# Optimization experiments

Hardware: AMD Instinct MI355X
Metric: run time of the kernel (lower is better)

## Reference

```python
import jax, jax.numpy as jnp
from jax import lax
import numpy as np

B, C2, H2, W2 = 16, 512, 28, 28
C3, H3, W3 = 1024, 14, 14
N_CORESET, EMB = 16384, C2 + C3
IMG = 224
NUM_NEIGHBORS = 9
SIGMA = 4.0
KS = 2 * int(4.0 * SIGMA + 0.5) + 1  # kornia default kernel size = 33


def setup_inputs() -> dict:
    key = jax.random.key(0)
    k1, k2, k3 = jax.random.split(key, 3)
    return {
        "feat_layer2": jax.random.normal(k1, (B, C2, H2, W2), jnp.float32),
        "feat_layer3": jax.random.normal(k2, (B, C3, H3, W3), jnp.float32),
        "embedding_coreset": jax.random.normal(k3, (N_CORESET, EMB), jnp.float32),
    }


def avg_pool3(x):
    # torch.nn.AvgPool2d(3, 1, 1), count_include_pad=True -> always divide by 9
    s = lax.reduce_window(x, 0.0, lax.add, (1, 1, 3, 3), (1, 1, 1, 1),
                          [(0, 0), (0, 0), (1, 1), (1, 1)])
    return s / 9.0


def cdist(a, b):
    # euclidean cdist: [Q,E] x [N,E] -> [Q,N]
    a2 = jnp.sum(a * a, axis=-1, keepdims=True)          # [Q,1]
    b2 = jnp.sum(b * b, axis=-1)[None, :]                # [1,N]
    d2 = a2 + b2 - 2.0 * (a @ b.T)
    return jnp.sqrt(jnp.maximum(d2, 1e-12))


def gaussian_blur(x):
    # kornia GaussianBlur2d(kernel=33, sigma=4, border='reflect'), separable
    half = (KS - 1) // 2
    t = jnp.arange(KS, dtype=x.dtype) - half
    k = jnp.exp(-(t * t) / (2.0 * SIGMA * SIGMA))
    k = k / jnp.sum(k)
    xp = jnp.pad(x, ((0, 0), (0, 0), (half, half), (half, half)), mode="reflect")
    dn = ("NCHW", "OIHW", "NCHW")
    y = lax.conv_general_dilated(xp, k.reshape(1, 1, KS, 1), (1, 1), "VALID", dimension_numbers=dn)
    y = lax.conv_general_dilated(y, k.reshape(1, 1, 1, KS), (1, 1), "VALID", dimension_numbers=dn)
    return y


def reference(feat_layer2, feat_layer3, embedding_coreset):
    # 1. feature pooling (AvgPool2d(3,1,1)) on each backbone layer
    p2 = avg_pool3(feat_layer2)                           # [B,512,28,28]
    p3 = avg_pool3(feat_layer3)                           # [B,1024,14,14]
    p3u = jnp.repeat(jnp.repeat(p3, 2, axis=2), 2, axis=3)  # [B,1024,28,28]
    embedding = jnp.concatenate([p2, p3u], axis=1)        # [B,1536,28,28]
    b, e, w, h = embedding.shape
    x = embedding.transpose(0, 2, 3, 1).reshape(-1, e)    # [B*28*28, 1536]

    # 3. nearest neighbor (n_neighbors=1) against the coreset
    dists = cdist(x, embedding_coreset)                   # [Q, N]
    patch_scores = jnp.min(dists, axis=1).reshape(b, -1)  # [B, P]
    locations = jnp.argmin(dists, axis=1).reshape(b, -1)  # [B, P]

    # 4. image-level anomaly score with num_neighbors=9 reweighting
    bidx = jnp.arange(b)
    max_patches = jnp.argmax(patch_scores, axis=1)        # [B]
    mpf = x.reshape(b, w * h, e)[bidx, max_patches]       # [B, E]
    score = patch_scores[bidx, max_patches]               # [B]
    nn_index = locations[bidx, max_patches]               # [B]
    nn_sample = embedding_coreset[nn_index]               # [B, E]
    d2 = cdist(nn_sample, embedding_coreset)              # [B, N]
    _, support = lax.top_k(-d2, NUM_NEIGHBORS)            # smallest 9, ascending
    sup_feats = embedding_coreset[support]                # [B, 9, E]
    diff = mpf[:, None, :] - sup_feats
    d_sup = jnp.sqrt(jnp.maximum(jnp.sum(diff * diff, axis=-1), 1e-12))  # [B, 9]
    weights = (1.0 - jax.nn.softmax(d_sup, axis=1))[:, 0]
    anomaly_score = weights * score                       # [B]

    # 5. anomaly map: bilinear upsample + gaussian blur
    sm = patch_scores.reshape(b, 1, w, h)
    sm = jax.image.resize(sm, (b, 1, IMG, IMG), method="bilinear")
    anomaly_map = gaussian_blur(sm)                       # [B,1,224,224]
    return anomaly_map, anomaly_score
```

## Files before the change

kernel.cpp:

```cpp
#include <hip/hip_runtime.h>
#include <math.h>

typedef unsigned char u8;
typedef unsigned short u16;
typedef unsigned int u32;
typedef unsigned long long u64;
typedef __attribute__((ext_vector_type(8))) int int8v;
typedef __attribute__((ext_vector_type(4))) int int4v;
typedef __attribute__((ext_vector_type(4))) float f32x4;

#define B_IMG 16
#define EMB 1536
#define NPATCH 784
#define Q_TOT (B_IMG * NPATCH)
#define NCORE 16384
#define BK 128
#define IMG 224
#define KS 33
#define HALF 16
#define REFINE_W 12.0f

#define BM 256
#define BN 256
#define MBLK (Q_TOT / BM)
#define NBLK2 (NCORE / BN)
#define NHALF 256
#define NKS (EMB / BK)


__device__ __forceinline__ u32 fkey(float f) {
    u32 u = __float_as_uint(f);
    return (u & 0x80000000u) ? ~u : (u | 0x80000000u);
}
__device__ __forceinline__ float fkey_inv(u32 k) {
    u32 u = (k & 0x80000000u) ? (k ^ 0x80000000u) : ~k;
    return __uint_as_float(u);
}

__device__ __forceinline__ u32 f2e4m3(float f) {
    u32 x = __float_as_uint(f);
    u32 sign = (x >> 24) & 0x80u;
    x &= 0x7fffffffu;
    if (x >= 0x43E00000u) return sign | 0x7Eu;
    u32 e = x >> 23;
    if (e >= 121) {
        u32 m = x & 0x7fffffu;
        u32 keep = m >> 20;
        u32 rest = m & 0xFFFFFu;
        u32 rnd = (rest > 0x80000u) || (rest == 0x80000u && (keep & 1u));
        u32 mant = keep + rnd;
        u32 e4 = e - 120;
        if (mant == 8) { mant = 0; e4 += 1; }
        return sign | (e4 << 3) | mant;
    }
    float a = __uint_as_float(x);
    u32 q = (u32)(a * 512.0f + 0.5f);
    if (q > 7) return sign | 0x08u;
    return sign | q;
}

__device__ __forceinline__ void async_copy16(const void* gsrc, void* ldst) {
    auto g = reinterpret_cast<const __attribute__((address_space(1))) u32*>(
        reinterpret_cast<uintptr_t>(gsrc));
    auto l = reinterpret_cast<__attribute__((address_space(3))) u32*>(
        reinterpret_cast<uintptr_t>(ldst));
    __builtin_amdgcn_global_load_lds(g, l, 16, 0, 0);
}

__global__ void k_split_cs(const float* __restrict__ cs, u8* __restrict__ cs8,
                           float* __restrict__ b2) {
    __shared__ float sm[4];
    const int n = blockIdx.x;
    const int t = threadIdx.x;
    const size_t base = (size_t)n * EMB;
    float s = 0.f;
#pragma unroll
    for (int i = 0; i < 6; ++i) {
        const int e = t + i * 256;
        float v = cs[base + e];
        cs8[base + e] = (u8)f2e4m3(v);
        s += v * v;
    }
#pragma unroll
    for (int off = 32; off > 0; off >>= 1) s += __shfl_down(s, off, 64);
    if ((t & 63) == 0) sm[t >> 6] = s;
    __syncthreads();
    if (t == 0) b2[n] = sm[0] + sm[1] + sm[2] + sm[3];
}

__global__ void k_build_x(const float* __restrict__ f2, const float* __restrict__ f3,
                          u8* __restrict__ x8, float* __restrict__ xf) {
    __shared__ float tile[32][33];
    const int tx = threadIdx.x, ty = threadIdx.y;
    const int hw0 = blockIdx.x * 32;
    const int e0 = blockIdx.y * 32;
    const int b = blockIdx.z;
    const int hw = hw0 + tx;
    const bool ok = hw < NPATCH;
    const int h = hw / 28, w = hw - h * 28;
#pragma unroll
    for (int j = 0; j < 4; ++j) {
        const int el = ty + 8 * j;
        const int e = e0 + el;
        float v = 0.f;
        if (ok) {
            if (e < 512) {
                const float* p = f2 + (size_t)(b * 512 + e) * 784;
#pragma unroll
                for (int dy = -1; dy <= 1; ++dy) {
                    int yy = h + dy;
                    if (yy < 0 || yy >= 28) continue;
#pragma unroll
                    for (int dx = -1; dx <= 1; ++dx) {
                        int xx = w + dx;
                        if (xx < 0 || xx >= 28) continue;
                        v += p[yy * 28 + xx];
                    }
                }
            } else {
                const int c = e - 512;
                const int y3 = h >> 1, x3 = w >> 1;
                const float* p = f3 + (size_t)(b * 1024 + c) * 196;
#pragma unroll
                for (int dy = -1; dy <= 1; ++dy) {
                    int yy = y3 + dy;
                    if (yy < 0 || yy >= 14) continue;
#pragma unroll
                    for (int dx = -1; dx <= 1; ++dx) {
                        int xx = x3 + dx;
                        if (xx < 0 || xx >= 14) continue;
                        v += p[yy * 14 + xx];
                    }
                }
            }
            v *= (1.0f / 9.0f);
        }
        tile[el][tx] = v;
    }
    __syncthreads();
#pragma unroll
    for (int j = 0; j < 4; ++j) {
        const int hwl = ty + 8 * j;
        const int hw2 = hw0 + hwl;
        if (hw2 < NPATCH) {
            const int q = b * NPATCH + hw2;
            const float v = tile[tx][hwl];
            x8[(size_t)q * EMB + e0 + tx] = (u8)f2e4m3(v);
            xf[(size_t)q * EMB + e0 + tx] = v;
        }
    }
}

__global__ __launch_bounds__(512, 2) void k_gemm(
    const u8* __restrict__ x8, const u8* __restrict__ cs8,
    const float* __restrict__ b2, u64* __restrict__ cand) {
    __shared__ __align__(16) u8 sA0[BM * BK];
    __shared__ __align__(16) u8 sA1[BM * BK];
    __shared__ __align__(16) u8 sB0[BN * BK];
    __shared__ __align__(16) u8 sB1[BN * BK];

    const int tid = threadIdx.x;
    const int lane = tid & 63;
    const int wid = tid >> 6;
    const int wy = wid >> 2;
    const int wx = wid & 3;
    const int qd = lane >> 4;
    const int lr = lane & 15;
    const int sw = lr & 7;

    const u32 bid = blockIdx.x;
    const u32 xcd = bid & 7;
    const u32 sl = bid >> 3;
    const int bx = (int)(xcd * 8 + (sl & 7));
    const int by = (int)(sl >> 3);
    const int m0 = by * BM;
    const int n0 = bx * BN;

    size_t srcA[4], srcB[4];
    int dst[4];
#pragma unroll
    for (int j = 0; j < 4; ++j) {
        const int s = tid + j * 512;
        const int r = s >> 3, p = s & 7;
        const int col = (p ^ (r & 7)) << 4;
        srcA[j] = (size_t)(m0 + r) * EMB + col;
        srcB[j] = (size_t)(n0 + r) * EMB + col;
        dst[j] = s << 4;
    }

    f32x4 acc[8][4];
#pragma unroll
    for (int i = 0; i < 8; ++i)
#pragma unroll
        for (int j = 0; j < 4; ++j) acc[i][j] = (f32x4){0.f, 0.f, 0.f, 0.f};

    const int aoff0 = (wy * 128 + lr) * BK + (((qd * 2) ^ sw) << 4);
    const int boff0 = (wx * 64 + lr) * BK + (((qd * 2) ^ sw) << 4);

#define STAGE(SA, SB, KSI) do {                                                \
        const size_t kk_ = (size_t)(KSI) * BK;                                 \
        _Pragma("unroll")                                                      \
        for (int j_ = 0; j_ < 4; ++j_) {                                       \
            async_copy16(x8 + srcA[j_] + kk_, (SA) + dst[j_]);                 \
            async_copy16(cs8 + srcB[j_] + kk_, (SB) + dst[j_]);                \
        }                                                                      \
    } while (0)

#define COMPUTE(SA, SB) do {                                                   \
        int8v a_[8];                                                           \
        _Pragma("unroll")                                                      \
        for (int mi_ = 0; mi_ < 8; ++mi_) {                                    \
            const int o_ = aoff0 + mi_ * (16 * BK);                            \
            *(int4v*)&a_[mi_] = *(const int4v*)((SA) + o_);                    \
            *(((int4v*)&a_[mi_]) + 1) = *(const int4v*)((SA) + (o_ ^ 16));     \
        }                                                                      \
        _Pragma("unroll")                                                      \
        for (int nj_ = 0; nj_ < 4; ++nj_) {                                    \
            const int ob_ = boff0 + nj_ * (16 * BK);                           \
            int8v b_;                                                          \
            *(int4v*)&b_ = *(const int4v*)((SB) + ob_);                        \
            *(((int4v*)&b_) + 1) = *(const int4v*)((SB) + (ob_ ^ 16));         \
            _Pragma("unroll")                                                  \
            for (int mi_ = 0; mi_ < 8; ++mi_)                                  \
                acc[mi_][nj_] = __builtin_amdgcn_mfma_scale_f32_16x16x128_f8f6f4( \
                    a_[mi_], b_, acc[mi_][nj_], 0, 0, 0, 0x7F7F7F7F, 0, 0x7F7F7F7F); \
        }                                                                      \
    } while (0)

    STAGE(sA0, sB0, 0);
    __syncthreads();
    for (int ks = 0; ks < NKS; ks += 2) {
        STAGE(sA1, sB1, ks + 1);
        COMPUTE(sA0, sB0);
        __syncthreads();
        if (ks + 2 < NKS) STAGE(sA0, sB0, ks + 2);
        COMPUTE(sA1, sB1);
        __syncthreads();
    }
#undef STAGE
#undef COMPUTE

    float bb[4];
#pragma unroll
    for (int nj = 0; nj < 4; ++nj) bb[nj] = b2[n0 + wx * 64 + nj * 16 + lr];

#pragma unroll
    for (int mi = 0; mi < 8; ++mi) {
#pragma unroll
        for (int r = 0; r < 4; ++r) {
            u64 best = ~0ull;
#pragma unroll
            for (int nj = 0; nj < 4; ++nj) {
                const int n_g = n0 + wx * 64 + nj * 16 + lr;
                float v = bb[nj] - 2.0f * acc[mi][nj][r];
                u64 key = ((u64)fkey(v) << 32) | (u32)n_g;
                best = best < key ? best : key;
            }
#pragma unroll
            for (int s = 1; s < 16; s <<= 1) {
                u64 o = __shfl_xor(best, s, 64);
                best = best < o ? best : o;
            }
            if (lr == 0) {
                const int m_l = wy * 128 + mi * 16 + qd * 4 + r;
                cand[(size_t)(m0 + m_l) * NHALF + (bx * 4 + wx)] = best;
            }
        }
    }
}

__global__ void k_refine(const u64* __restrict__ cand, const float* __restrict__ xf,
                         const float* __restrict__ cs,
                         float* __restrict__ scores, int* __restrict__ locs) {
    __shared__ float sx[EMB];
    __shared__ float wred_f[4];
    __shared__ u64 wred_u[4];
    __shared__ u64 wbest_s[4];
    __shared__ int clist[16];
    __shared__ int ccount;
    __shared__ float s_a2, s_lim;
    const int row = blockIdx.x;
    const int t = threadIdx.x;
    const int lane = t & 63, wv = t >> 6;

    const u64 mykey = cand[(size_t)row * NHALF + t];
    float p = 0.f;
    for (int e = t; e < EMB; e += 256) {
        float v = xf[(size_t)row * EMB + e];
        sx[e] = v;
        p += v * v;
    }
    if (t == 0) ccount = 0;
#pragma unroll
    for (int off = 32; off > 0; off >>= 1) p += __shfl_down(p, off, 64);
    u64 kmin = mykey;
#pragma unroll
    for (int s = 1; s < 64; s <<= 1) {
        u64 o = __shfl_xor(kmin, s, 64);
        kmin = o < kmin ? o : kmin;
    }
    if (lane == 0) { wred_f[wv] = p; wred_u[wv] = kmin; }
    __syncthreads();
    if (t == 0) {
        float a2 = wred_f[0] + wred_f[1] + wred_f[2] + wred_f[3];
        u64 km = wred_u[0];
        km = wred_u[1] < km ? wred_u[1] : km;
        km = wred_u[2] < km ? wred_u[2] : km;
        km = wred_u[3] < km ? wred_u[3] : km;
        s_a2 = a2;
        s_lim = a2 + fkey_inv((u32)(km >> 32)) + REFINE_W;
    }
    __syncthreads();
    {
        float d2a = s_a2 + fkey_inv((u32)(mykey >> 32));
        if (d2a <= s_lim) {
            int pos = atomicAdd(&ccount, 1);
            if (pos < 16) clist[pos] = (int)(mykey & 0xffffffffu);
        }
    }
    __syncthreads();
    const int nc = min(ccount, 16);
    u64 wb = ~0ull;
    for (int i = wv; i < nc; i += 4) {
        const int n = clist[i];
        const float* c = cs + (size_t)n * EMB;
        float q = 0.f;
        for (int e = lane; e < EMB; e += 64) {
            float d = sx[e] - c[e];
            q += d * d;
        }
#pragma unroll
        for (int off = 32; off > 0; off >>= 1) q += __shfl_down(q, off, 64);
        if (lane == 0) {
            u64 key = ((u64)fkey(q) << 32) | (u32)n;
            wb = wb < key ? wb : key;
        }
    }
    if (lane == 0) wbest_s[wv] = wb;
    __syncthreads();
    if (t == 0) {
        u64 best = wbest_s[0];
        best = wbest_s[1] < best ? wbest_s[1] : best;
        best = wbest_s[2] < best ? wbest_s[2] : best;
        best = wbest_s[3] < best ? wbest_s[3] : best;
        float d2 = fkey_inv((u32)(best >> 32));
        scores[row] = sqrtf(fmaxf(d2, 1e-12f));
        locs[row] = (int)(best & 0xffffffffu);
    }
}

__global__ void k_argmax(const float* __restrict__ scores, const int* __restrict__ locs,
                         float* __restrict__ imgscore, int* __restrict__ nnidx,
                         int* __restrict__ qstar) {
    __shared__ u64 red[4];
    const int b = blockIdx.x, t = threadIdx.x;
    const int lane = t & 63, wv = t >> 6;
    u64 best = 0;
    for (int p = t; p < NPATCH; p += 256) {
        u32 u = __float_as_uint(scores[b * NPATCH + p]);
        u64 key = ((u64)u << 32) | (u32)(0xFFFFFFFFu - (u32)p);
        best = best > key ? best : key;
    }
#pragma unroll
    for (int s = 1; s < 64; s <<= 1) {
        u64 o = __shfl_xor(best, s, 64);
        best = o > best ? o : best;
    }
    if (lane == 0) red[wv] = best;
    __syncthreads();
    if (t == 0) {
        u64 k = red[0];
        k = red[1] > k ? red[1] : k;
        k = red[2] > k ? red[2] : k;
        k = red[3] > k ? red[3] : k;
        int p = (int)(0xFFFFFFFFu - (u32)(k & 0xFFFFFFFFu));
        imgscore[b] = __uint_as_float((u32)(k >> 32));
        nnidx[b] = locs[b * NPATCH + p];
        qstar[b] = b * NPATCH + p;
    }
}

__global__ void k_d2nn(const float* __restrict__ cs, const int* __restrict__ nnidx,
                       float* __restrict__ dpart) {
    __shared__ float snn[16 * 384];
    const int t = threadIdx.x;
    const int nb = blockIdx.x & 63, ksl = blockIdx.x >> 6;
    const int n = nb * 256 + t;
    const int k0 = ksl * 384;
#pragma unroll
    for (int j = 0; j < 6; ++j) {
        int fid = t + j * 256;
        int row = fid / 96;
        int c4 = fid - row * 96;
        ((float4*)snn)[row * 96 + c4] =
            ((const float4*)(cs + (size_t)nnidx[row] * EMB + k0))[c4];
    }
    __syncthreads();
    float acc[16];
#pragma unroll
    for (int b = 0; b < 16; ++b) acc[b] = 0.f;
    const float4* csrow = (const float4*)(cs + (size_t)n * EMB + k0);
    for (int k4 = 0; k4 < 96; ++k4) {
        float4 c4 = csrow[k4];
#pragma unroll
        for (int b = 0; b < 16; ++b) {
            float4 nb4 = ((const float4*)snn)[b * 96 + k4];
            acc[b] += c4.x * nb4.x + c4.y * nb4.y + c4.z * nb4.z + c4.w * nb4.w;
        }
    }
#pragma unroll
    for (int b = 0; b < 16; ++b)
        dpart[((size_t)ksl * 16 + b) * NCORE + n] = acc[b];
}

__global__ void k_topk(const float* __restrict__ dpart, const float* __restrict__ b2,
                       const int* __restrict__ nnidx,
                       const float* __restrict__ cs, const float* __restrict__ xf,
                       const int* __restrict__ qstar, const float* __restrict__ imgscore,
                       float* __restrict__ out_scores) {
    __shared__ float sd2[NCORE];
    __shared__ float sxq[EMB];
    __shared__ int sel_idx[9];
    __shared__ float dsup[9];
    __shared__ u64 wred[4];
    const int b = blockIdx.x, t = threadIdx.x;
    const int lane = t & 63, wv = t >> 6;
    const float bnn = b2[nnidx[b]];
    const int q = qstar[b];
    for (int n = t; n < NCORE; n += 256) {
        float dot = dpart[(0 * 16 + b) * NCORE + n] + dpart[(1 * 16 + b) * NCORE + n] +
                    dpart[(2 * 16 + b) * NCORE + n] + dpart[(3 * 16 + b) * NCORE + n];
        sd2[n] = bnn + b2[n] - 2.f * dot;
    }
    for (int e = t; e < EMB; e += 256) sxq[e] = xf[(size_t)q * EMB + e];
    __syncthreads();

    for (int j = 0; j < 9; ++j) {
        u64 best = ~0ull;
        for (int n = t; n < NCORE; n += 256) {
            u64 key = ((u64)fkey(sd2[n]) << 32) | (u32)n;
            best = best < key ? best : key;
        }
#pragma unroll
        for (int s = 1; s < 64; s <<= 1) {
            u64 o = __shfl_xor(best, s, 64);
            best = o < best ? o : best;
        }
        if (lane == 0) wred[wv] = best;
        __syncthreads();
        if (t == 0) {
            u64 k0 = wred[0];
            k0 = wred[1] < k0 ? wred[1] : k0;
            k0 = wred[2] < k0 ? wred[2] : k0;
            k0 = wred[3] < k0 ? wred[3] : k0;
            int sel = (int)(k0 & 0xffffffffu);
            sel_idx[j] = sel;
            sd2[sel] = __uint_as_float(0x7F800000u);
        }
        __syncthreads();
    }

    for (int j = wv; j < 9; j += 4) {
        const int s = sel_idx[j];
        const float* c = cs + (size_t)s * EMB;
        float p = 0.f;
        for (int e = lane; e < EMB; e += 64) {
            float d = sxq[e] - c[e];
            p += d * d;
        }
#pragma unroll
        for (int off = 32; off > 0; off >>= 1) p += __shfl_down(p, off, 64);
        if (lane == 0) dsup[j] = sqrtf(fmaxf(p, 1e-12f));
    }
    __syncthreads();

    if (t == 0) {
        float m = dsup[0];
        for (int j = 1; j < 9; ++j) m = fmaxf(m, dsup[j]);
        float se = 0.f, e0 = 0.f;
        for (int j = 0; j < 9; ++j) {
            float e = expf(dsup[j] - m);
            se += e;
            if (j == 0) e0 = e;
        }
        out_scores[b] = (1.0f - e0 / se) * imgscore[b];
    }
}

__global__ void k_bilx(const float* __restrict__ scores, float* __restrict__ Sx) {
    int i = blockIdx.x * 256 + threadIdx.x;
    if (i >= B_IMG * 28 * IMG) return;
    int x = i % IMG;
    int br = i / IMG;
    int r = br % 28, b = br / 28;
    float cx = (x + 0.5f) * 0.125f - 0.5f;
    int x0 = (int)floorf(cx);
    float fx = cx - (float)x0;
    int x1 = min(max(x0 + 1, 0), 27);
    x0 = min(max(x0, 0), 27);
    const float* s = scores + b * NPATCH + r * 28;
    Sx[i] = (1.f - fx) * s[x0] + fx * s[x1];
}

__global__ void k_blur_vf(const float* __restrict__ Sx, float* __restrict__ out1) {
    __shared__ float wv[28];
    const int y = blockIdx.x, b = blockIdx.y, t = threadIdx.x;
    if (t < 28) wv[t] = 0.f;
    __syncthreads();
    if (t == 0) {
        float wsum = 0.f;
        for (int j = 0; j < KS; ++j) {
            float d = (float)(j - HALF);
            wsum += expf(-(d * d) / 32.0f);
        }
        for (int j = 0; j < KS; ++j) {
            int yy = y - HALF + j;
            yy = yy < 0 ? -yy : (yy > 223 ? 446 - yy : yy);
            float cy = (yy + 0.5f) * 0.125f - 0.5f;
            int y0 = (int)floorf(cy);
            float fy = cy - (float)y0;
            int y1 = min(max(y0 + 1, 0), 27);
            y0 = min(max(y0, 0), 27);
            float d = (float)(j - HALF);
            float wkj = expf(-(d * d) / 32.0f) / wsum;
            wv[y0] += (1.f - fy) * wkj;
            wv[y1] += fy * wkj;
        }
    }
    __syncthreads();
    if (t < IMG) {
        float acc = 0.f;
#pragma unroll
        for (int r = 0; r < 28; ++r) acc += wv[r] * Sx[(b * 28 + r) * IMG + t];
        out1[((size_t)b * IMG + y) * IMG + t] = acc;
    }
}

__global__ void k_blur_h(const float* __restrict__ out1, float* __restrict__ out) {
    __shared__ float row[IMG];
    __shared__ float wk[KS];
    const int y = blockIdx.x, b = blockIdx.y, t = threadIdx.x;
    if (t < IMG) row[t] = out1[((size_t)b * IMG + y) * IMG + t];
    if (t < KS) {
        float d = (float)(t - HALF);
        wk[t] = expf(-(d * d) / 32.0f);
    }
    __syncthreads();
    if (t < IMG) {
        float wsum = 0.f, acc = 0.f;
#pragma unroll
        for (int j = 0; j < KS; ++j) wsum += wk[j];
#pragma unroll
        for (int j = 0; j < KS; ++j) {
            int xx = t - HALF + j;
            xx = xx < 0 ? -xx : (xx > 223 ? 446 - xx : xx);
            acc += wk[j] * row[xx];
        }
        out[((size_t)b * IMG + y) * IMG + t] = acc / wsum;
    }
}

extern "C" void kernel_launch(void* const* d_in, const int* in_sizes, int n_in,
                              void* d_out, int out_size, void* d_ws, size_t ws_size,
                              hipStream_t stream) {
    const float* f2 = (const float*)d_in[0];
    const float* f3 = (const float*)d_in[1];
    const float* cs = (const float*)d_in[2];
    float* out = (float*)d_out;

    char* w = (char*)d_ws;
    auto alloc = [&](size_t bytes) {
        char* p = w;
        w += (bytes + 255) & ~(size_t)255;
        return p;
    };
    u8* x8 = (u8*)alloc((size_t)Q_TOT * EMB);
    float* xf = (float*)alloc((size_t)Q_TOT * EMB * 4);
    u8* cs8 = (u8*)alloc((size_t)NCORE * EMB);
    float* b2 = (float*)alloc(NCORE * 4);
    u64* cand = (u64*)alloc((size_t)Q_TOT * NHALF * 8);
    float* scores = (float*)alloc(Q_TOT * 4);
    int* locs = (int*)alloc(Q_TOT * 4);
    float* imgscore = (float*)alloc(B_IMG * 4);
    int* nnidx = (int*)alloc(B_IMG * 4);
    int* qstar = (int*)alloc(B_IMG * 4);
    float* dpart = (float*)alloc((size_t)4 * B_IMG * NCORE * 4);
    float* Sx = (float*)alloc((size_t)B_IMG * 28 * IMG * 4);
    float* map1 = (float*)alloc((size_t)B_IMG * IMG * IMG * 4);

    k_split_cs<<<NCORE, 256, 0, stream>>>(cs, cs8, b2);
    k_build_x<<<dim3(25, 48, 16), dim3(32, 8), 0, stream>>>(f2, f3, x8, xf);
    k_gemm<<<dim3(MBLK * NBLK2), 512, 0, stream>>>(x8, cs8, b2, cand);
    k_refine<<<Q_TOT, 256, 0, stream>>>(cand, xf, cs, scores, locs);
    k_argmax<<<16, 256, 0, stream>>>(scores, locs, imgscore, nnidx, qstar);
    k_d2nn<<<256, 256, 0, stream>>>(cs, nnidx, dpart);
    k_topk<<<16, 256, 0, stream>>>(dpart, b2, nnidx, cs, xf, qstar, imgscore,
                                   out + B_IMG * IMG * IMG);
    k_bilx<<<(B_IMG * 28 * IMG + 255) / 256, 256, 0, stream>>>(scores, Sx);
    k_blur_vf<<<dim3(IMG, B_IMG), 256, 0, stream>>>(Sx, map1);
    k_blur_h<<<dim3(IMG, B_IMG), 256, 0, stream>>>(map1, out);
}
```

Before: 1.047 ms.

## Fuse prep kernels, fold argmax into refine via atomics, merge anomaly-map kernels

Merges the coreset-quantise and embedding-build kernels into one launch. The per-image argmax moves into k_refine through a 64-bit atomicMax on a packed score/index key, so the k_argmax kernel goes away. The bilinear and two blur kernels become one k_amap kernel that keeps its intermediates in shared memory instead of global buffers. This cuts launch count and global traffic for intermediates, at the cost of per-block recomputation of the horizontal bilinear row in k_amap and atomic contention on 16 keys.

```diff
diff --git a/kernel.cpp b/kernel.cpp
--- a/kernel.cpp
+++ b/kernel.cpp
@@ -67,34 +67,41 @@
     __builtin_amdgcn_global_load_lds(g, l, 16, 0, 0);
 }
 
-__global__ void k_split_cs(const float* __restrict__ cs, u8* __restrict__ cs8,
-                           float* __restrict__ b2) {
+__global__ void k_prep(const float* __restrict__ cs, const float* __restrict__ f2,
+                       const float* __restrict__ f3, u8* __restrict__ cs8,
+                       float* __restrict__ b2, u8* __restrict__ x8,
+                       float* __restrict__ xf, u64* __restrict__ imgkey) {
     __shared__ float sm[4];
-    const int n = blockIdx.x;
+    __shared__ float tile[32][33];
+    const int bid = blockIdx.x;
     const int t = threadIdx.x;
-    const size_t base = (size_t)n * EMB;
-    float s = 0.f;
-#pragma unroll
-    for (int i = 0; i < 6; ++i) {
-        const int e = t + i * 256;
-        float v = cs[base + e];
-        cs8[base + e] = (u8)f2e4m3(v);
-        s += v * v;
-    }
-#pragma unroll
-    for (int off = 32; off > 0; off >>= 1) s += __shfl_down(s, off, 64);
-    if ((t & 63) == 0) sm[t >> 6] = s;
-    __syncthreads();
-    if (t == 0) b2[n] = sm[0] + sm[1] + sm[2] + sm[3];
-}
-
-__global__ void k_build_x(const float* __restrict__ f2, const float* __restrict__ f3,
-                          u8* __restrict__ x8, float* __restrict__ xf) {
-    __shared__ float tile[32][33];
-    const int tx = threadIdx.x, ty = threadIdx.y;
-    const int hw0 = blockIdx.x * 32;
-    const int e0 = blockIdx.y * 32;
-    const int b = blockIdx.z;
+    if (bid < NCORE) {
+        if (bid == 0 && t < B_IMG) imgkey[t] = 0ull;
+        const int n = bid;
+        const size_t base = (size_t)n * EMB;
+        float s = 0.f;
+#pragma unroll
+        for (int i = 0; i < 6; ++i) {
+            const int e = t + i * 256;
+            float v = cs[base + e];
+            cs8[base + e] = (u8)f2e4m3(v);
+            s += v * v;
+        }
+#pragma unroll
+        for (int off = 32; off > 0; off >>= 1) s += __shfl_down(s, off, 64);
+        if ((t & 63) == 0) sm[t >> 6] = s;
+        __syncthreads();
+        if (t == 0) b2[n] = sm[0] + sm[1] + sm[2] + sm[3];
+        return;
+    }
+    const int bid2 = bid - NCORE;
+    const int bxx = bid2 % 25;
+    const int byy = (bid2 / 25) % 48;
+    const int bzz = bid2 / (25 * 48);
+    const int tx = t & 31, ty = t >> 5;
+    const int hw0 = bxx * 32;
+    const int e0 = byy * 32;
+    const int b = bzz;
     const int hw = hw0 + tx;
     const bool ok = hw < NPATCH;
     const int h = hw / 28, w = hw - h * 28;
@@ -271,7 +278,8 @@
 
 __global__ void k_refine(const u64* __restrict__ cand, const float* __restrict__ xf,
                          const float* __restrict__ cs,
-                         float* __restrict__ scores, int* __restrict__ locs) {
+                         float* __restrict__ scores, int* __restrict__ locs,
+                         u64* __restrict__ imgkey) {
     __shared__ float sx[EMB];
     __shared__ float wred_f[4];
     __shared__ u64 wred_u[4];
@@ -344,56 +352,37 @@
         best = wbest_s[2] < best ? wbest_s[2] : best;
         best = wbest_s[3] < best ? wbest_s[3] : best;
         float d2 = fkey_inv((u32)(best >> 32));
-        scores[row] = sqrtf(fmaxf(d2, 1e-12f));
+        float sc = sqrtf(fmaxf(d2, 1e-12f));
+        scores[row] = sc;
         locs[row] = (int)(best & 0xffffffffu);
-    }
-}
-
-__global__ void k_argmax(const float* __restrict__ scores, const int* __restrict__ locs,
-                         float* __restrict__ imgscore, int* __restrict__ nnidx,
-                         int* __restrict__ qstar) {
-    __shared__ u64 red[4];
-    const int b = blockIdx.x, t = threadIdx.x;
-    const int lane = t & 63, wv = t >> 6;
-    u64 best = 0;
-    for (int p = t; p < NPATCH; p += 256) {
-        u32 u = __float_as_uint(scores[b * NPATCH + p]);
-        u64 key = ((u64)u << 32) | (u32)(0xFFFFFFFFu - (u32)p);
-        best = best > key ? best : key;
-    }
-#pragma unroll
-    for (int s = 1; s < 64; s <<= 1) {
-        u64 o = __shfl_xor(best, s, 64);
-        best = o > best ? o : best;
-    }
-    if (lane == 0) red[wv] = best;
-    __syncthreads();
-    if (t == 0) {
-        u64 k = red[0];
-        k = red[1] > k ? red[1] : k;
-        k = red[2] > k ? red[2] : k;
-        k = red[3] > k ? red[3] : k;
-        int p = (int)(0xFFFFFFFFu - (u32)(k & 0xFFFFFFFFu));
-        imgscore[b] = __uint_as_float((u32)(k >> 32));
-        nnidx[b] = locs[b * NPATCH + p];
-        qstar[b] = b * NPATCH + p;
-    }
-}
-
-__global__ void k_d2nn(const float* __restrict__ cs, const int* __restrict__ nnidx,
-                       float* __restrict__ dpart) {
+        const int b = row / NPATCH;
+        const int pp = row - b * NPATCH;
+        u64 akey = ((u64)__float_as_uint(sc) << 32) | (u32)(0xFFFFFFFFu - (u32)pp);
+        atomicMax((unsigned long long*)&imgkey[b], (unsigned long long)akey);
+    }
+}
+
+__global__ void k_d2nn(const float* __restrict__ cs, const u64* __restrict__ imgkey,
+                       const int* __restrict__ locs, float* __restrict__ dpart) {
     __shared__ float snn[16 * 384];
+    __shared__ int snn_idx[16];
     const int t = threadIdx.x;
     const int nb = blockIdx.x & 63, ksl = blockIdx.x >> 6;
     const int n = nb * 256 + t;
     const int k0 = ksl * 384;
+    if (t < 16) {
+        u64 k = imgkey[t];
+        int p = (int)(0xFFFFFFFFu - (u32)(k & 0xFFFFFFFFu));
+        snn_idx[t] = locs[t * NPATCH + p];
+    }
+    __syncthreads();
 #pragma unroll
     for (int j = 0; j < 6; ++j) {
         int fid = t + j * 256;
         int row = fid / 96;
         int c4 = fid - row * 96;
         ((float4*)snn)[row * 96 + c4] =
-            ((const float4*)(cs + (size_t)nnidx[row] * EMB + k0))[c4];
+            ((const float4*)(cs + (size_t)snn_idx[row] * EMB + k0))[c4];
     }
     __syncthreads();
     float acc[16];
@@ -414,9 +403,8 @@
 }
 
 __global__ void k_topk(const float* __restrict__ dpart, const float* __restrict__ b2,
-                       const int* __restrict__ nnidx,
+                       const u64* __restrict__ imgkey, const int* __restrict__ locs,
                        const float* __restrict__ cs, const float* __restrict__ xf,
-                       const int* __restrict__ qstar, const float* __restrict__ imgscore,
                        float* __restrict__ out_scores) {
     __shared__ float sd2[NCORE];
     __shared__ float sxq[EMB];
@@ -425,8 +413,12 @@
     __shared__ u64 wred[4];
     const int b = blockIdx.x, t = threadIdx.x;
     const int lane = t & 63, wv = t >> 6;
-    const float bnn = b2[nnidx[b]];
-    const int q = qstar[b];
+    const u64 ik = imgkey[b];
+    const int pp = (int)(0xFFFFFFFFu - (u32)(ik & 0xFFFFFFFFu));
+    const int q = b * NPATCH + pp;
+    const int nn = locs[q];
+    const float bnn = b2[nn];
+    const float imgsc = __uint_as_float((u32)(ik >> 32));
     for (int n = t; n < NCORE; n += 256) {
         float dot = dpart[(0 * 16 + b) * NCORE + n] + dpart[(1 * 16 + b) * NCORE + n] +
                     dpart[(2 * 16 + b) * NCORE + n] + dpart[(3 * 16 + b) * NCORE + n];
@@ -483,36 +475,38 @@
             se += e;
             if (j == 0) e0 = e;
         }
-        out_scores[b] = (1.0f - e0 / se) * imgscore[b];
-    }
-}
-
-__global__ void k_bilx(const float* __restrict__ scores, float* __restrict__ Sx) {
-    int i = blockIdx.x * 256 + threadIdx.x;
-    if (i >= B_IMG * 28 * IMG) return;
-    int x = i % IMG;
-    int br = i / IMG;
-    int r = br % 28, b = br / 28;
-    float cx = (x + 0.5f) * 0.125f - 0.5f;
-    int x0 = (int)floorf(cx);
-    float fx = cx - (float)x0;
-    int x1 = min(max(x0 + 1, 0), 27);
-    x0 = min(max(x0, 0), 27);
-    const float* s = scores + b * NPATCH + r * 28;
-    Sx[i] = (1.f - fx) * s[x0] + fx * s[x1];
-}
-
-__global__ void k_blur_vf(const float* __restrict__ Sx, float* __restrict__ out1) {
-    __shared__ float wv[28];
+        out_scores[b] = (1.0f - e0 / se) * imgsc;
+    }
+}
+
+__global__ void k_amap(const float* __restrict__ scores, float* __restrict__ out) {
+    __shared__ float ss[NPATCH];
+    __shared__ float sxr[28][IMG];
+    __shared__ float vrow[IMG];
+    __shared__ float wk[KS];
+    __shared__ float wvv[28];
+    __shared__ float swsum;
     const int y = blockIdx.x, b = blockIdx.y, t = threadIdx.x;
-    if (t < 28) wv[t] = 0.f;
-    __syncthreads();
+    for (int i = t; i < NPATCH; i += 256) ss[i] = scores[b * NPATCH + i];
+    if (t < KS) {
+        float d = (float)(t - HALF);
+        wk[t] = expf(-(d * d) / 32.0f);
+    }
+    if (t < 28) wvv[t] = 0.f;
+    __syncthreads();
+    for (int i = t; i < 28 * IMG; i += 256) {
+        int r = i / IMG, x = i - r * IMG;
+        float cx = (x + 0.5f) * 0.125f - 0.5f;
+        int x0 = (int)floorf(cx);
+        float fx = cx - (float)x0;
+        int x1 = min(max(x0 + 1, 0), 27);
+        x0 = min(max(x0, 0), 27);
+        sxr[r][x] = (1.f - fx) * ss[r * 28 + x0] + fx * ss[r * 28 + x1];
+    }
     if (t == 0) {
         float wsum = 0.f;
-        for (int j = 0; j < KS; ++j) {
-            float d = (float)(j - HALF);
-            wsum += expf(-(d * d) / 32.0f);
-        }
+        for (int j = 0; j < KS; ++j) wsum += wk[j];
+        swsum = wsum;
         for (int j = 0; j < KS; ++j) {
             int yy = y - HALF + j;
             yy = yy < 0 ? -yy : (yy > 223 ? 446 - yy : yy);
@@ -521,42 +515,28 @@
             float fy = cy - (float)y0;
             int y1 = min(max(y0 + 1, 0), 27);
             y0 = min(max(y0, 0), 27);
-            float d = (float)(j - HALF);
-            float wkj = expf(-(d * d) / 32.0f) / wsum;
-            wv[y0] += (1.f - fy) * wkj;
-            wv[y1] += fy * wkj;
-        }
+            float wkj = wk[j] / wsum;
+            wvv[y0] += (1.f - fy) * wkj;
+            wvv[y1] += fy * wkj;
+        }
+    }
+    __syncthreads();
+    if (t < IMG) {
+        float a = 0.f;
+#pragma unroll
+        for (int r = 0; r < 28; ++r) a += wvv[r] * sxr[r][t];
+        vrow[t] = a;
     }
     __syncthreads();
     if (t < IMG) {
         float acc = 0.f;
-#pragma unroll
-        for (int r = 0; r < 28; ++r) acc += wv[r] * Sx[(b * 28 + r) * IMG + t];
-        out1[((size_t)b * IMG + y) * IMG + t] = acc;
-    }
-}
-
-__global__ void k_blur_h(const float* __restrict__ out1, float* __restrict__ out) {
-    __shared__ float row[IMG];
-    __shared__ float wk[KS];
-    const int y = blockIdx.x, b = blockIdx.y, t = threadIdx.x;
-    if (t < IMG) row[t] = out1[((size_t)b * IMG + y) * IMG + t];
-    if (t < KS) {
-        float d = (float)(t - HALF);
-        wk[t] = expf(-(d * d) / 32.0f);
-    }
-    __syncthreads();
-    if (t < IMG) {
-        float wsum = 0.f, acc = 0.f;
-#pragma unroll
-        for (int j = 0; j < KS; ++j) wsum += wk[j];
 #pragma unroll
         for (int j = 0; j < KS; ++j) {
             int xx = t - HALF + j;
             xx = xx < 0 ? -xx : (xx > 223 ? 446 - xx : xx);
-            acc += wk[j] * row[xx];
-        }
-        out[((size_t)b * IMG + y) * IMG + t] = acc / wsum;
+            acc += wk[j] * vrow[xx];
+        }
+        out[((size_t)b * IMG + y) * IMG + t] = acc / swsum;
     }
 }
 
@@ -581,22 +561,15 @@
     u64* cand = (u64*)alloc((size_t)Q_TOT * NHALF * 8);
     float* scores = (float*)alloc(Q_TOT * 4);
     int* locs = (int*)alloc(Q_TOT * 4);
-    float* imgscore = (float*)alloc(B_IMG * 4);
-    int* nnidx = (int*)alloc(B_IMG * 4);
-    int* qstar = (int*)alloc(B_IMG * 4);
+    u64* imgkey = (u64*)alloc(B_IMG * 8);
     float* dpart = (float*)alloc((size_t)4 * B_IMG * NCORE * 4);
-    float* Sx = (float*)alloc((size_t)B_IMG * 28 * IMG * 4);
-    float* map1 = (float*)alloc((size_t)B_IMG * IMG * IMG * 4);
-
-    k_split_cs<<<NCORE, 256, 0, stream>>>(cs, cs8, b2);
-    k_build_x<<<dim3(25, 48, 16), dim3(32, 8), 0, stream>>>(f2, f3, x8, xf);
+
+    k_prep<<<NCORE + 25 * 48 * 16, 256, 0, stream>>>(cs, f2, f3, cs8, b2, x8, xf,
+                                                     imgkey);
     k_gemm<<<dim3(MBLK * NBLK2), 512, 0, stream>>>(x8, cs8, b2, cand);
-    k_refine<<<Q_TOT, 256, 0, stream>>>(cand, xf, cs, scores, locs);
-    k_argmax<<<16, 256, 0, stream>>>(scores, locs, imgscore, nnidx, qstar);
-    k_d2nn<<<256, 256, 0, stream>>>(cs, nnidx, dpart);
-    k_topk<<<16, 256, 0, stream>>>(dpart, b2, nnidx, cs, xf, qstar, imgscore,
+    k_refine<<<Q_TOT, 256, 0, stream>>>(cand, xf, cs, scores, locs, imgkey);
+    k_d2nn<<<256, 256, 0, stream>>>(cs, imgkey, locs, dpart);
+    k_topk<<<16, 256, 0, stream>>>(dpart, b2, imgkey, locs, cs, xf,
                                    out + B_IMG * IMG * IMG);
-    k_bilx<<<(B_IMG * 28 * IMG + 255) / 256, 256, 0, stream>>>(scores, Sx);
-    k_blur_vf<<<dim3(IMG, B_IMG), 256, 0, stream>>>(Sx, map1);
-    k_blur_h<<<dim3(IMG, B_IMG), 256, 0, stream>>>(map1, out);
-}
+    k_amap<<<dim3(IMG, B_IMG), 256, 0, stream>>>(scores, out);
+}
```

Measured after the change: 1.091 ms. 1.04x slower.
